# Performance work log

Measured on AMD Instinct MI355X. Metric: run time of the kernel, lower is better.

## Reference

```python
import jax, jax.numpy as jnp
import numpy as np


def _per_sample_ce(logits, targets):
    # -log_softmax(logits)[i, targets[i]]  -> shape [N]
    logp = jax.nn.log_softmax(logits, axis=-1)
    return -jnp.take_along_axis(logp, targets[:, None], axis=-1)[:, 0]


def setup_inputs() -> dict:
    key = jax.random.key(0)
    k1, k2, k3 = jax.random.split(key, 3)
    N, C = 65536, 1000
    y_1 = jax.random.normal(k1, (N, C), dtype=jnp.float32)
    y_2 = jax.random.normal(k2, (N, C), dtype=jnp.float32)
    targets = jax.random.randint(k3, (N,), 0, C, dtype=jnp.int64)
    num_keep = 45875  # int(0.7 * N), static for jit
    return {"y_1": y_1, "y_2": y_2, "targets": targets, "num_keep": num_keep}


def reference(y_1, y_2, targets, num_keep):
    loss_1 = _per_sample_ce(y_1, targets)          # [N]
    loss_2 = _per_sample_ce(y_2, targets)          # [N]
    # small-loss selection: indices of the num_keep smallest per-sample losses
    ind_1_update = jnp.argsort(loss_1)[:num_keep]  # selected by net 1
    ind_2_update = jnp.argsort(loss_2)[:num_keep]  # selected by net 2
    # cross-update: each net trains on the peer's selected samples
    loss_1_update = _per_sample_ce(y_1[ind_2_update], targets[ind_2_update])
    loss_2_update = _per_sample_ce(y_2[ind_1_update], targets[ind_1_update])
    # size_average=True -> means
    return (loss_1_update.mean(), loss_2_update.mean(),
            loss_1.mean(), loss_2.mean())
```

## Files before the change

### kernel.cpp

```cpp
#include <hip/hip_runtime.h>
#include <math.h>

#define MAXT 2048

__device__ __forceinline__ unsigned keyOf(float f) {
  unsigned b = __float_as_uint(f);
  return b ^ ((b & 0x80000000u) ? 0xFFFFFFFFu : 0x80000000u);
}

__device__ __forceinline__ float waveSum(float v) {
#pragma unroll
  for (int o = 32; o >= 1; o >>= 1) v += __shfl_xor(v, o);
  return v;
}

__device__ __forceinline__ void selectStep(const unsigned* __restrict__ h,
                                           int per, unsigned rank,
                                           unsigned* sc, unsigned* res) {
  int t = threadIdx.x;
  unsigned local[8];
  unsigned s = 0;
  for (int j = 0; j < per; ++j) { local[j] = h[t * per + j]; s += local[j]; }
  sc[t] = s;
  __syncthreads();
  for (int off = 1; off < 256; off <<= 1) {
    unsigned v = (t >= off) ? sc[t - off] : 0u;
    __syncthreads();
    sc[t] += v;
    __syncthreads();
  }
  unsigned incl = sc[t], excl = incl - s;
  if (excl < rank && rank <= incl) {
    unsigned cum = excl;
    for (int j = 0; j < per; ++j) {
      if (cum + local[j] >= rank) {
        res[0] = (unsigned)(t * per + j);
        res[1] = rank - cum;
        break;
      }
      cum += local[j];
    }
  }
  __syncthreads();
}

__global__ __launch_bounds__(256) void ce_kernel(
    const float* __restrict__ y1, const float* __restrict__ y2,
    const int* __restrict__ tgt,
    float* __restrict__ l1, float* __restrict__ l2,
    unsigned* __restrict__ zeroBase, int zeroCount, int N) {
  const float L2E = 1.4426950408889634f;
  const float LN2 = 0.6931471805599453f;
  if (blockIdx.x == 0) {
    for (int j = threadIdx.x; j < zeroCount; j += 256) zeroBase[j] = 0u;
  }
  int wid = threadIdx.x >> 6, lane = threadIdx.x & 63;
  int row = blockIdx.x * 4 + wid;
  if (row >= N) return;
  int t = tgt[row];
  int vecIdx = t >> 2;
  int grp = vecIdx >> 6;
  int srcLane = vecIdx & 63;
  int comp = t & 3;
  const float4* rp1 = (const float4*)(y1 + (size_t)row * 1000);
  const float4* rp2 = (const float4*)(y2 + (size_t)row * 1000);
  float4 a1 = rp1[lane];
  float4 b1 = rp1[lane + 64];
  float4 c1 = rp1[lane + 128];
  float4 a2 = rp2[lane];
  float4 b2 = rp2[lane + 64];
  float4 c2 = rp2[lane + 128];
  float4 d1 = make_float4(-INFINITY, -INFINITY, -INFINITY, -INFINITY);
  float4 d2 = d1;
  if (lane < 58) {
    d1 = rp1[lane + 192];
    d2 = rp2[lane + 192];
  }
  float4 sel1 = (grp == 0) ? a1 : (grp == 1) ? b1 : (grp == 2) ? c1 : d1;
  float4 sel2 = (grp == 0) ? a2 : (grp == 1) ? b2 : (grp == 2) ? c2 : d2;
  float cand1 = (comp == 0) ? sel1.x : (comp == 1) ? sel1.y
              : (comp == 2) ? sel1.z : sel1.w;
  float cand2 = (comp == 0) ? sel2.x : (comp == 1) ? sel2.y
              : (comp == 2) ? sel2.z : sel2.w;
  float xt1 = __shfl(cand1, srcLane);
  float xt2 = __shfl(cand2, srcLane);
#define E_(v) exp2f((v) * L2E)
  float s1 = (((E_(a1.x) + E_(a1.y)) + (E_(a1.z) + E_(a1.w))) +
              ((E_(b1.x) + E_(b1.y)) + (E_(b1.z) + E_(b1.w)))) +
             (((E_(c1.x) + E_(c1.y)) + (E_(c1.z) + E_(c1.w))) +
              ((E_(d1.x) + E_(d1.y)) + (E_(d1.z) + E_(d1.w))));
  float s2 = (((E_(a2.x) + E_(a2.y)) + (E_(a2.z) + E_(a2.w))) +
              ((E_(b2.x) + E_(b2.y)) + (E_(b2.z) + E_(b2.w)))) +
             (((E_(c2.x) + E_(c2.y)) + (E_(c2.z) + E_(c2.w))) +
              ((E_(d2.x) + E_(d2.y)) + (E_(d2.z) + E_(d2.w))));
#undef E_
#pragma unroll
  for (int o = 32; o >= 1; o >>= 1) {
    s1 += __shfl_xor(s1, o);
    s2 += __shfl_xor(s2, o);
  }
  if (lane == 0) {
    l1[row] = log2f(s1) * LN2 - xt1;
    l2[row] = log2f(s2) * LN2 - xt2;
  }
}

__global__ __launch_bounds__(256) void histA_kernel(
    const float* __restrict__ l1, const float* __restrict__ l2,
    unsigned* __restrict__ hA1, unsigned* __restrict__ hA2, int N) {
  __shared__ unsigned lh[2][2048];
  int t = threadIdx.x;
  for (int j = t; j < 2048; j += 256) { lh[0][j] = 0u; lh[1][j] = 0u; }
  __syncthreads();
  for (int i = blockIdx.x * blockDim.x + t; i < N;
       i += gridDim.x * blockDim.x) {
    atomicAdd(&lh[0][keyOf(l1[i]) >> 21], 1u);
    atomicAdd(&lh[1][keyOf(l2[i]) >> 21], 1u);
  }
  __syncthreads();
  for (int j = t; j < 2048; j += 256) {
    unsigned v0 = lh[0][j], v1 = lh[1][j];
    if (v0) atomicAdd(&hA1[j], v0);
    if (v1) atomicAdd(&hA2[j], v1);
  }
}

__global__ __launch_bounds__(256) void histB_kernel(
    const float* __restrict__ l1, const float* __restrict__ l2,
    const unsigned* __restrict__ hA1, const unsigned* __restrict__ hA2,
    unsigned* __restrict__ hB1, unsigned* __restrict__ hB2,
    const int* __restrict__ numKeep, int N) {
  __shared__ unsigned sc[256];
  __shared__ unsigned resA1[2], resA2[2];
  unsigned k0 = (unsigned)(*numKeep);
  selectStep(hA1, 8, k0, sc, resA1);
  selectStep(hA2, 8, k0, sc, resA2);
  unsigned a1 = resA1[0], a2 = resA2[0];
  for (int i = blockIdx.x * blockDim.x + threadIdx.x; i < N;
       i += gridDim.x * blockDim.x) {
    unsigned k1 = keyOf(l1[i]);
    if ((k1 >> 21) == a1) atomicAdd(&hB1[(k1 >> 10) & 2047u], 1u);
    unsigned k2 = keyOf(l2[i]);
    if ((k2 >> 21) == a2) atomicAdd(&hB2[(k2 >> 10) & 2047u], 1u);
  }
}

__global__ __launch_bounds__(256) void partial_kernel(
    const float* __restrict__ l1, const float* __restrict__ l2,
    const unsigned* __restrict__ hA1, const unsigned* __restrict__ hA2,
    const unsigned* __restrict__ hB1, const unsigned* __restrict__ hB2,
    const int* __restrict__ numKeep, unsigned* __restrict__ tc,
    unsigned* __restrict__ done,
    int* __restrict__ tIdx1, unsigned* __restrict__ tKey1, float* __restrict__ tVal1,
    int* __restrict__ tIdx2, unsigned* __restrict__ tKey2, float* __restrict__ tVal2,
    float* __restrict__ partials, float* __restrict__ out, int N) {
  __shared__ unsigned sc[256];
  __shared__ unsigned rA1[2], rA2[2], rB1[2], rB2[2];
  unsigned k0 = (unsigned)(*numKeep);
  selectStep(hA1, 8, k0, sc, rA1);
  selectStep(hA2, 8, k0, sc, rA2);
  selectStep(hB1, 8, rA1[1], sc, rB1);
  selectStep(hB2, 8, rA2[1], sc, rB2);
  unsigned P1 = (rA1[0] << 11) | rB1[0];
  unsigned P2 = (rA2[0] << 11) | rB2[0];
  float s0 = 0.f, s1 = 0.f, s2 = 0.f, s3 = 0.f;
  for (int i = blockIdx.x * blockDim.x + threadIdx.x; i < N;
       i += gridDim.x * blockDim.x) {
    float f1 = l1[i], f2 = l2[i];
    unsigned k1 = keyOf(f1), k2 = keyOf(f2);
    unsigned q1 = k1 >> 10, q2 = k2 >> 10;
    if (q2 < P2) {
      s0 += f1;
    } else if (q2 == P2) {
      unsigned p = atomicAdd(&tc[1], 1u);
      if (p < MAXT) { tIdx2[p] = i; tKey2[p] = k2; tVal2[p] = f1; }
    }
    if (q1 < P1) {
      s1 += f2;
    } else if (q1 == P1) {
      unsigned p = atomicAdd(&tc[0], 1u);
      if (p < MAXT) { tIdx1[p] = i; tKey1[p] = k1; tVal1[p] = f2; }
    }
    s2 += f1;
    s3 += f2;
  }
  s0 = waveSum(s0); s1 = waveSum(s1); s2 = waveSum(s2); s3 = waveSum(s3);
  __shared__ float red[4][4];
  int wid = threadIdx.x >> 6, lane = threadIdx.x & 63;
  if (lane == 0) {
    red[wid][0] = s0; red[wid][1] = s1; red[wid][2] = s2; red[wid][3] = s3;
  }
  __syncthreads();
  if (threadIdx.x == 0) {
    for (int q = 0; q < 4; ++q)
      partials[blockIdx.x * 4 + q] =
          red[0][q] + red[1][q] + red[2][q] + red[3][q];
  }
  __shared__ unsigned amLast;
  __threadfence();
  if (threadIdx.x == 0)
    amLast = (atomicAdd(done, 1u) == (unsigned)(gridDim.x - 1)) ? 1u : 0u;
  __syncthreads();
  if (!amLast) return;
  __threadfence();
  int t = threadIdx.x;
  float u0 = 0.f, u1 = 0.f, u2 = 0.f, u3 = 0.f;
  for (int j = t; j < (int)gridDim.x; j += 256) {
    u0 += partials[j * 4 + 0];
    u1 += partials[j * 4 + 1];
    u2 += partials[j * 4 + 2];
    u3 += partials[j * 4 + 3];
  }
  u0 = waveSum(u0); u1 = waveSum(u1); u2 = waveSum(u2); u3 = waveSum(u3);
  __syncthreads();
  if (lane == 0) {
    red[wid][0] = u0; red[wid][1] = u1; red[wid][2] = u2; red[wid][3] = u3;
  }
  __shared__ float slots[MAXT];
  __shared__ float tieSum[2];
  unsigned needArr[2] = {rB1[1], rB2[1]};
  for (int a = 0; a < 2; ++a) {
    const int* ti = a ? tIdx2 : tIdx1;
    const unsigned* tk = a ? tKey2 : tKey1;
    const float* tv = a ? tVal2 : tVal1;
    int T = min((int)tc[a], MAXT);
    int need = min((int)needArr[a], T);
    __syncthreads();
    for (int j = t; j < T; j += 256) {
      int idx = ti[j];
      unsigned kj = tk[j];
      int rk = 0;
      for (int m = 0; m < T; ++m) {
        unsigned km = tk[m];
        rk += (km < kj || (km == kj && ti[m] < idx)) ? 1 : 0;
      }
      if (rk < need) slots[rk] = tv[j];
    }
    __syncthreads();
    if (t == 0) {
      float s = 0.f;
      for (int j = 0; j < need; ++j) s += slots[j];
      tieSum[a] = s;
    }
  }
  __syncthreads();
  if (t == 0) {
    float a0 = red[0][0] + red[1][0] + red[2][0] + red[3][0] + tieSum[1];
    float a1 = red[0][1] + red[1][1] + red[2][1] + red[3][1] + tieSum[0];
    float a2 = red[0][2] + red[1][2] + red[2][2] + red[3][2];
    float a3 = red[0][3] + red[1][3] + red[2][3] + red[3][3];
    float k = (float)k0;
    out[0] = a0 / k;
    out[1] = a1 / k;
    out[2] = a2 / (float)N;
    out[3] = a3 / (float)N;
  }
}

extern "C" void kernel_launch(void* const* d_in, const int* in_sizes, int n_in,
                              void* d_out, int out_size, void* d_ws,
                              size_t ws_size, hipStream_t stream) {
  const float* y1 = (const float*)d_in[0];
  const float* y2 = (const float*)d_in[1];
  const int* tgt = (const int*)d_in[2];
  const int* numKeep = (const int*)d_in[3];
  int N = in_sizes[2];
  float* out = (float*)d_out;

  float* l1 = (float*)d_ws;
  float* l2 = l1 + N;
  unsigned* hA1 = (unsigned*)(l2 + N);
  unsigned* hA2 = hA1 + 2048;
  unsigned* hB1 = hA2 + 2048;
  unsigned* hB2 = hB1 + 2048;
  unsigned* tc = hB2 + 2048;
  unsigned* done = tc + 2;
  int* tIdx1 = (int*)(done + 1);
  unsigned* tKey1 = (unsigned*)(tIdx1 + MAXT);
  float* tVal1 = (float*)(tKey1 + MAXT);
  int* tIdx2 = (int*)(tVal1 + MAXT);
  unsigned* tKey2 = (unsigned*)(tIdx2 + MAXT);
  float* tVal2 = (float*)(tKey2 + MAXT);
  float* partials = (float*)(tVal2 + MAXT);

  ce_kernel<<<(N + 3) / 4, 256, 0, stream>>>(y1, y2, tgt, l1, l2, hA1,
                                             4 * 2048 + 3, N);
  histA_kernel<<<256, 256, 0, stream>>>(l1, l2, hA1, hA2, N);
  histB_kernel<<<256, 256, 0, stream>>>(l1, l2, hA1, hA2, hB1, hB2, numKeep, N);
  partial_kernel<<<256, 256, 0, stream>>>(l1, l2, hA1, hA2, hB1, hB2, numKeep,
                                          tc, done, tIdx1, tKey1, tVal1, tIdx2,
                                          tKey2, tVal2, partials, out, N);
}
```

Baseline: 144.8 us.

## Make CE kernel persistent with software-prefetched rows, one wave per net-row

```diff
diff --git a/kernel.cpp b/kernel.cpp
--- a/kernel.cpp
+++ b/kernel.cpp
@@ -44,65 +44,61 @@
   __syncthreads();
 }
 
+__device__ __forceinline__ void ceFinish(int row, int t, int lane,
+                                         float4 a, float4 b, float4 c,
+                                         float4 d, float* __restrict__ L) {
+  const float L2E = 1.4426950408889634f;
+  const float LN2 = 0.6931471805599453f;
+  int vecIdx = t >> 2;
+  int grp = vecIdx >> 6, srcLane = vecIdx & 63, comp = t & 3;
+  float4 sel = (grp == 0) ? a : (grp == 1) ? b : (grp == 2) ? c : d;
+  float cand = (comp == 0) ? sel.x : (comp == 1) ? sel.y
+             : (comp == 2) ? sel.z : sel.w;
+  float xt = __shfl(cand, srcLane);
+#define E_(v) exp2f((v) * L2E)
+  float s = (((E_(a.x) + E_(a.y)) + (E_(a.z) + E_(a.w))) +
+             ((E_(b.x) + E_(b.y)) + (E_(b.z) + E_(b.w)))) +
+            (((E_(c.x) + E_(c.y)) + (E_(c.z) + E_(c.w))) +
+             ((E_(d.x) + E_(d.y)) + (E_(d.z) + E_(d.w))));
+#undef E_
+  s = waveSum(s);
+  if (lane == 0) L[row] = log2f(s) * LN2 - xt;
+}
+
 __global__ __launch_bounds__(256) void ce_kernel(
     const float* __restrict__ y1, const float* __restrict__ y2,
     const int* __restrict__ tgt,
     float* __restrict__ l1, float* __restrict__ l2,
     unsigned* __restrict__ zeroBase, int zeroCount, int N) {
-  const float L2E = 1.4426950408889634f;
-  const float LN2 = 0.6931471805599453f;
   if (blockIdx.x == 0) {
     for (int j = threadIdx.x; j < zeroCount; j += 256) zeroBase[j] = 0u;
   }
   int wid = threadIdx.x >> 6, lane = threadIdx.x & 63;
-  int row = blockIdx.x * 4 + wid;
-  if (row >= N) return;
-  int t = tgt[row];
-  int vecIdx = t >> 2;
-  int grp = vecIdx >> 6;
-  int srcLane = vecIdx & 63;
-  int comp = t & 3;
-  const float4* rp1 = (const float4*)(y1 + (size_t)row * 1000);
-  const float4* rp2 = (const float4*)(y2 + (size_t)row * 1000);
-  float4 a1 = rp1[lane];
-  float4 b1 = rp1[lane + 64];
-  float4 c1 = rp1[lane + 128];
-  float4 a2 = rp2[lane];
-  float4 b2 = rp2[lane + 64];
-  float4 c2 = rp2[lane + 128];
-  float4 d1 = make_float4(-INFINITY, -INFINITY, -INFINITY, -INFINITY);
-  float4 d2 = d1;
-  if (lane < 58) {
-    d1 = rp1[lane + 192];
-    d2 = rp2[lane + 192];
-  }
-  float4 sel1 = (grp == 0) ? a1 : (grp == 1) ? b1 : (grp == 2) ? c1 : d1;
-  float4 sel2 = (grp == 0) ? a2 : (grp == 1) ? b2 : (grp == 2) ? c2 : d2;
-  float cand1 = (comp == 0) ? sel1.x : (comp == 1) ? sel1.y
-              : (comp == 2) ? sel1.z : sel1.w;
-  float cand2 = (comp == 0) ? sel2.x : (comp == 1) ? sel2.y
-              : (comp == 2) ? sel2.z : sel2.w;
-  float xt1 = __shfl(cand1, srcLane);
-  float xt2 = __shfl(cand2, srcLane);
-#define E_(v) exp2f((v) * L2E)
-  float s1 = (((E_(a1.x) + E_(a1.y)) + (E_(a1.z) + E_(a1.w))) +
-              ((E_(b1.x) + E_(b1.y)) + (E_(b1.z) + E_(b1.w)))) +
-             (((E_(c1.x) + E_(c1.y)) + (E_(c1.z) + E_(c1.w))) +
-              ((E_(d1.x) + E_(d1.y)) + (E_(d1.z) + E_(d1.w))));
-  float s2 = (((E_(a2.x) + E_(a2.y)) + (E_(a2.z) + E_(a2.w))) +
-              ((E_(b2.x) + E_(b2.y)) + (E_(b2.z) + E_(b2.w)))) +
-             (((E_(c2.x) + E_(c2.y)) + (E_(c2.z) + E_(c2.w))) +
-              ((E_(d2.x) + E_(d2.y)) + (E_(d2.z) + E_(d2.w))));
-#undef E_
-#pragma unroll
-  for (int o = 32; o >= 1; o >>= 1) {
-    s1 += __shfl_xor(s1, o);
-    s2 += __shfl_xor(s2, o);
-  }
-  if (lane == 0) {
-    l1[row] = log2f(s1) * LN2 - xt1;
-    l2[row] = log2f(s2) * LN2 - xt2;
-  }
+  int w = blockIdx.x * 4 + wid;
+  int nWaves = gridDim.x * 4;
+  int net = w & 1;
+  int r = w >> 1;
+  int rstride = nWaves >> 1;
+  if (r >= N) return;
+  const float* Y = net ? y2 : y1;
+  float* L = net ? l2 : l1;
+  const float4 negInf = make_float4(-INFINITY, -INFINITY, -INFINITY, -INFINITY);
+  int dOff = (lane < 58) ? (lane + 192) : 249;
+
+  const float4* p = (const float4*)(Y + (size_t)r * 1000);
+  int ct = tgt[r];
+  float4 a = p[lane], b = p[lane + 64], c = p[lane + 128], d = p[dOff];
+  if (lane >= 58) d = negInf;
+
+  for (int rn = r + rstride; rn < N; rn += rstride) {
+    const float4* q = (const float4*)(Y + (size_t)rn * 1000);
+    int nt = tgt[rn];
+    float4 na = q[lane], nb = q[lane + 64], nc = q[lane + 128], nd = q[dOff];
+    if (lane >= 58) nd = negInf;
+    ceFinish(r, ct, lane, a, b, c, d, L);
+    a = na; b = nb; c = nc; d = nd; ct = nt; r = rn;
+  }
+  ceFinish(r, ct, lane, a, b, c, d, L);
 }
 
 __global__ __launch_bounds__(256) void histA_kernel(
@@ -283,8 +279,8 @@
   float* tVal2 = (float*)(tKey2 + MAXT);
   float* partials = (float*)(tVal2 + MAXT);
 
-  ce_kernel<<<(N + 3) / 4, 256, 0, stream>>>(y1, y2, tgt, l1, l2, hA1,
-                                             4 * 2048 + 3, N);
+  ce_kernel<<<2048, 256, 0, stream>>>(y1, y2, tgt, l1, l2, hA1,
+                                      4 * 2048 + 3, N);
   histA_kernel<<<256, 256, 0, stream>>>(l1, l2, hA1, hA2, N);
   histB_kernel<<<256, 256, 0, stream>>>(l1, l2, hA1, hA2, hB1, hB2, numKeep, N);
   partial_kernel<<<256, 256, 0, stream>>>(l1, l2, hA1, hA2, hB1, hB2, numKeep,
```

Result: slower. 149.9 us (+3.5%).

## Fuse histogram, refine, and partial-sum kernels into one cooperative kernel

Applied to the files above, without the earlier changes.

```diff
diff --git a/kernel.cpp b/kernel.cpp
--- a/kernel.cpp
+++ b/kernel.cpp
@@ -1,5 +1,8 @@
 #include <hip/hip_runtime.h>
+#include <hip/hip_cooperative_groups.h>
 #include <math.h>
+
+namespace cg = cooperative_groups;
 
 #define MAXT 2048
 
@@ -47,13 +50,9 @@
 __global__ __launch_bounds__(256) void ce_kernel(
     const float* __restrict__ y1, const float* __restrict__ y2,
     const int* __restrict__ tgt,
-    float* __restrict__ l1, float* __restrict__ l2,
-    unsigned* __restrict__ zeroBase, int zeroCount, int N) {
+    float* __restrict__ l1, float* __restrict__ l2, int N) {
   const float L2E = 1.4426950408889634f;
   const float LN2 = 0.6931471805599453f;
-  if (blockIdx.x == 0) {
-    for (int j = threadIdx.x; j < zeroCount; j += 256) zeroBase[j] = 0u;
-  }
   int wid = threadIdx.x >> 6, lane = threadIdx.x & 63;
   int row = blockIdx.x * 4 + wid;
   if (row >= N) return;
@@ -105,15 +104,29 @@
   }
 }
 
-__global__ __launch_bounds__(256) void histA_kernel(
+__global__ __launch_bounds__(256) void tail_kernel(
     const float* __restrict__ l1, const float* __restrict__ l2,
-    unsigned* __restrict__ hA1, unsigned* __restrict__ hA2, int N) {
+    unsigned* __restrict__ hA1, unsigned* __restrict__ hA2,
+    unsigned* __restrict__ hB1, unsigned* __restrict__ hB2,
+    unsigned* __restrict__ tc,
+    int* __restrict__ tIdx1, unsigned* __restrict__ tKey1,
+    float* __restrict__ tVal1,
+    int* __restrict__ tIdx2, unsigned* __restrict__ tKey2,
+    float* __restrict__ tVal2,
+    float* __restrict__ partials, const int* __restrict__ numKeep,
+    float* __restrict__ out, int N) {
+  cg::grid_group grid = cg::this_grid();
+  int t = threadIdx.x;
+  int gid = blockIdx.x * 256 + t;
+  int gsize = gridDim.x * 256;
+
+  for (int j = gid; j < 4 * 2048 + 2; j += gsize) hA1[j] = 0u;
+  grid.sync();
+
   __shared__ unsigned lh[2][2048];
-  int t = threadIdx.x;
   for (int j = t; j < 2048; j += 256) { lh[0][j] = 0u; lh[1][j] = 0u; }
   __syncthreads();
-  for (int i = blockIdx.x * blockDim.x + t; i < N;
-       i += gridDim.x * blockDim.x) {
+  for (int i = gid; i < N; i += gsize) {
     atomicAdd(&lh[0][keyOf(l1[i]) >> 21], 1u);
     atomicAdd(&lh[1][keyOf(l2[i]) >> 21], 1u);
   }
@@ -123,49 +136,27 @@
     if (v0) atomicAdd(&hA1[j], v0);
     if (v1) atomicAdd(&hA2[j], v1);
   }
-}
-
-__global__ __launch_bounds__(256) void histB_kernel(
-    const float* __restrict__ l1, const float* __restrict__ l2,
-    const unsigned* __restrict__ hA1, const unsigned* __restrict__ hA2,
-    unsigned* __restrict__ hB1, unsigned* __restrict__ hB2,
-    const int* __restrict__ numKeep, int N) {
-  __shared__ unsigned sc[256];
-  __shared__ unsigned resA1[2], resA2[2];
-  unsigned k0 = (unsigned)(*numKeep);
-  selectStep(hA1, 8, k0, sc, resA1);
-  selectStep(hA2, 8, k0, sc, resA2);
-  unsigned a1 = resA1[0], a2 = resA2[0];
-  for (int i = blockIdx.x * blockDim.x + threadIdx.x; i < N;
-       i += gridDim.x * blockDim.x) {
-    unsigned k1 = keyOf(l1[i]);
-    if ((k1 >> 21) == a1) atomicAdd(&hB1[(k1 >> 10) & 2047u], 1u);
-    unsigned k2 = keyOf(l2[i]);
-    if ((k2 >> 21) == a2) atomicAdd(&hB2[(k2 >> 10) & 2047u], 1u);
-  }
-}
-
-__global__ __launch_bounds__(256) void partial_kernel(
-    const float* __restrict__ l1, const float* __restrict__ l2,
-    const unsigned* __restrict__ hA1, const unsigned* __restrict__ hA2,
-    const unsigned* __restrict__ hB1, const unsigned* __restrict__ hB2,
-    const int* __restrict__ numKeep, unsigned* __restrict__ tc,
-    unsigned* __restrict__ done,
-    int* __restrict__ tIdx1, unsigned* __restrict__ tKey1, float* __restrict__ tVal1,
-    int* __restrict__ tIdx2, unsigned* __restrict__ tKey2, float* __restrict__ tVal2,
-    float* __restrict__ partials, float* __restrict__ out, int N) {
+  grid.sync();
+
   __shared__ unsigned sc[256];
   __shared__ unsigned rA1[2], rA2[2], rB1[2], rB2[2];
   unsigned k0 = (unsigned)(*numKeep);
   selectStep(hA1, 8, k0, sc, rA1);
   selectStep(hA2, 8, k0, sc, rA2);
+  for (int i = gid; i < N; i += gsize) {
+    unsigned k1 = keyOf(l1[i]);
+    if ((k1 >> 21) == rA1[0]) atomicAdd(&hB1[(k1 >> 10) & 2047u], 1u);
+    unsigned k2 = keyOf(l2[i]);
+    if ((k2 >> 21) == rA2[0]) atomicAdd(&hB2[(k2 >> 10) & 2047u], 1u);
+  }
+  grid.sync();
+
   selectStep(hB1, 8, rA1[1], sc, rB1);
   selectStep(hB2, 8, rA2[1], sc, rB2);
   unsigned P1 = (rA1[0] << 11) | rB1[0];
   unsigned P2 = (rA2[0] << 11) | rB2[0];
   float s0 = 0.f, s1 = 0.f, s2 = 0.f, s3 = 0.f;
-  for (int i = blockIdx.x * blockDim.x + threadIdx.x; i < N;
-       i += gridDim.x * blockDim.x) {
+  for (int i = gid; i < N; i += gsize) {
     float f1 = l1[i], f2 = l2[i];
     unsigned k1 = keyOf(f1), k2 = keyOf(f2);
     unsigned q1 = k1 >> 10, q2 = k2 >> 10;
@@ -186,24 +177,19 @@
   }
   s0 = waveSum(s0); s1 = waveSum(s1); s2 = waveSum(s2); s3 = waveSum(s3);
   __shared__ float red[4][4];
-  int wid = threadIdx.x >> 6, lane = threadIdx.x & 63;
+  int wid = t >> 6, lane = t & 63;
   if (lane == 0) {
     red[wid][0] = s0; red[wid][1] = s1; red[wid][2] = s2; red[wid][3] = s3;
   }
   __syncthreads();
-  if (threadIdx.x == 0) {
+  if (t == 0) {
     for (int q = 0; q < 4; ++q)
       partials[blockIdx.x * 4 + q] =
           red[0][q] + red[1][q] + red[2][q] + red[3][q];
   }
-  __shared__ unsigned amLast;
-  __threadfence();
-  if (threadIdx.x == 0)
-    amLast = (atomicAdd(done, 1u) == (unsigned)(gridDim.x - 1)) ? 1u : 0u;
-  __syncthreads();
-  if (!amLast) return;
-  __threadfence();
-  int t = threadIdx.x;
+  grid.sync();
+
+  if (blockIdx.x != 0) return;
   float u0 = 0.f, u1 = 0.f, u2 = 0.f, u3 = 0.f;
   for (int j = t; j < (int)gridDim.x; j += 256) {
     u0 += partials[j * 4 + 0];
@@ -274,8 +260,7 @@
   unsigned* hB1 = hA2 + 2048;
   unsigned* hB2 = hB1 + 2048;
   unsigned* tc = hB2 + 2048;
-  unsigned* done = tc + 2;
-  int* tIdx1 = (int*)(done + 1);
+  int* tIdx1 = (int*)(tc + 2);
   unsigned* tKey1 = (unsigned*)(tIdx1 + MAXT);
   float* tVal1 = (float*)(tKey1 + MAXT);
   int* tIdx2 = (int*)(tVal1 + MAXT);
@@ -283,11 +268,13 @@
   float* tVal2 = (float*)(tKey2 + MAXT);
   float* partials = (float*)(tVal2 + MAXT);
 
-  ce_kernel<<<(N + 3) / 4, 256, 0, stream>>>(y1, y2, tgt, l1, l2, hA1,
-                                             4 * 2048 + 3, N);
-  histA_kernel<<<256, 256, 0, stream>>>(l1, l2, hA1, hA2, N);
-  histB_kernel<<<256, 256, 0, stream>>>(l1, l2, hA1, hA2, hB1, hB2, numKeep, N);
-  partial_kernel<<<256, 256, 0, stream>>>(l1, l2, hA1, hA2, hB1, hB2, numKeep,
-                                          tc, done, tIdx1, tKey1, tVal1, tIdx2,
-                                          tKey2, tVal2, partials, out, N);
-}
+  ce_kernel<<<(N + 3) / 4, 256, 0, stream>>>(y1, y2, tgt, l1, l2, N);
+
+  void* args[] = {(void*)&l1,    (void*)&l2,    (void*)&hA1,  (void*)&hA2,
+                  (void*)&hB1,   (void*)&hB2,   (void*)&tc,   (void*)&tIdx1,
+                  (void*)&tKey1, (void*)&tVal1, (void*)&tIdx2, (void*)&tKey2,
+                  (void*)&tVal2, (void*)&partials, (void*)&numKeep,
+                  (void*)&out,   (void*)&N};
+  hipLaunchCooperativeKernel((const void*)tail_kernel, dim3(256), dim3(256),
+                             args, 0, stream);
+}
```

Result: slower. 216.8 us (+49.7%).
